# Optimization experiments

Hardware: AMD Instinct MI355X
Metric: run time of the kernel (lower is better)

Reference implementation:

```python
import jax, jax.numpy as jnp
import numpy as np

TRAJ_NUM = 8
EVAL = 30
SGM_T = 2.0
D0 = 0.5
R = 0.3
VOX = 0.2


def setup_inputs() -> dict:
    key = jax.random.key(0)
    ks = jax.random.split(key, 6)
    G, M = 256, 4
    B = G * TRAJ_NUM
    nx, ny, nz = 400, 400, 64
    # quintic boundary matrix at t=0 and t=T; L = A^{-1}
    T = SGM_T
    A = np.array([
        [1, 0, 0, 0, 0, 0],
        [0, 1, 0, 0, 0, 0],
        [0, 0, 2, 0, 0, 0],
        [1, T, T**2, T**3, T**4, T**5],
        [0, 1, 2*T, 3*T**2, 4*T**3, 5*T**4],
        [0, 0, 2, 6*T, 12*T**2, 20*T**3]], dtype=np.float64)
    L = jnp.asarray(np.linalg.inv(A), dtype=jnp.float32)

    def state(k):
        kp, kv, ka = jax.random.split(k, 3)
        # positions inside the 80m x 80m x 12.8m map, away from borders
        p = jax.random.uniform(kp, (B, 3)) * jnp.array([70.0, 70.0, 10.0]) + jnp.array([5.0, 5.0, 1.0])
        v = jax.random.uniform(kv, (B, 3), minval=-1.0, maxval=1.0)
        a = jax.random.uniform(ka, (B, 3), minval=-0.5, maxval=0.5)
        return jnp.stack([p, v, a], axis=-1)  # (B,3,3): rows=axis, cols=[p,v,a]

    Df = state(ks[0])
    Dp = state(ks[1])
    sdf_maps = jax.random.normal(ks[2], (M, nz, ny, nx), dtype=jnp.float32) * 0.5 + 1.0  # (M,D,H,W)
    min_bounds = jnp.zeros((M, 3), jnp.float32)
    sdf_shapes = jnp.tile(jnp.array([[nx, ny, nz]], jnp.float32), (M, 1))  # (nx,ny,nz)
    map_id = jax.random.randint(ks[3], (G,), 0, M)
    return dict(Df=Df, Dp=Dp, L=L, sdf_maps=sdf_maps, min_bounds=min_bounds,
                sdf_shapes=sdf_shapes, map_id=map_id)


def _distance_cost(pos, map_id, sdf_maps, min_bounds, sdf_shapes):
    # pos: (G,N,3) world coords; replicates get_batch_sdf + grid_sample math
    mb = min_bounds[map_id]                           # (G,3)
    shp = sdf_shapes[map_id].astype(jnp.int32)        # (G,3) = (nx,ny,nz)
    mn = jnp.trunc((pos.min(1) - mb) / VOX).astype(jnp.int32)
    mx = jnp.trunc((pos.max(1) - mb) / VOX).astype(jnp.int32)
    max_spans = (mx - mn).max(0)                      # (3,) shared crop span
    c = (mn + mx) // 2
    mn = c - max_spans // 2 - 5
    mx = c + max_spans // 2 + 5
    nmn = jnp.maximum(mn, 0)
    mx = mx + (nmn - mn)
    mn = nmn
    nmx = jnp.minimum(mx, shp)
    mn = mn - (mx - nmx)
    mx = nmx
    shift = jnp.maximum(-jnp.minimum(mn, 0), 0).max(0)  # per-axis over batch
    mn = mn + shift
    local_origin = mn.astype(pos.dtype) * VOX + mb     # (G,3)
    lshape = mx - mn                                   # (G,3) int, crop size

    grid = (pos - local_origin[:, None, :]) / VOX      # local voxel coords (x,y,z)
    gp = 2.0 * grid / (lshape - 1).astype(pos.dtype)[:, None, :] - 1.0
    valid = jnp.all((gp < 0.99) & (gp > -0.99), axis=-1)  # (G,N)

    # trilinear sample, align_corners=True, zeros padding w.r.t. the crop;
    # crop voxel (i,j,k) == full-map voxel (i,j,k)+mn, so gather from the full map
    l0 = jnp.floor(grid).astype(jnp.int32)
    f = grid - l0
    Dm, Hm, Wm = sdf_maps.shape[1:]
    acc = jnp.zeros(pos.shape[:2], pos.dtype)
    for dx in (0, 1):
        for dy in (0, 1):
            for dz in (0, 1):
                il = l0 + jnp.array([dx, dy, dz], jnp.int32)       # (G,N,3) local corner
                inb = jnp.all((il >= 0) & (il < lshape[:, None, :]), axis=-1)
                ig = il + mn[:, None, :]                            # global voxel index
                gx = jnp.clip(ig[..., 0], 0, Wm - 1)
                gy = jnp.clip(ig[..., 1], 0, Hm - 1)
                gz = jnp.clip(ig[..., 2], 0, Dm - 1)
                val = sdf_maps[map_id[:, None], gz, gy, gx]         # (G,N)
                w = ((f[..., 0] if dx else 1 - f[..., 0]) *
                     (f[..., 1] if dy else 1 - f[..., 1]) *
                     (f[..., 2] if dz else 1 - f[..., 2]))
                acc = acc + jnp.where(inb, w * val, 0.0)
    dist = acc
    cost = jnp.exp(-(dist - D0) / R)
    cost = jnp.where(valid, cost, 0.0)
    return cost, dist


def reference(Df, Dp, L, sdf_maps, min_bounds, sdf_shapes, map_id):
    B = Dp.shape[0]
    # coefficients: per axis, coe = L @ [Df_row, Dp_row]
    d = jnp.concatenate([Df, Dp], axis=-1)          # (B,3,6)
    coe = jnp.einsum('jk,bik->bij', L, d)           # (B,3,6)
    dt = SGM_T / EVAL
    t = jnp.linspace(dt, SGM_T, EVAL)               # (30,)
    tp = t[:, None] ** jnp.arange(6)                # (30,6) Vandermonde
    pos = jnp.einsum('nk,bik->bni', tp, coe)        # (B,30,3)
    G = B // TRAJ_NUM
    pos_batch = pos.reshape(G, TRAJ_NUM * EVAL, 3)  # (G,N,3)
    cost, _ = _distance_cost(pos_batch, map_id, sdf_maps, min_bounds, sdf_shapes)
    cost_colli = (cost * dt).reshape(-1, EVAL).sum(-1)  # (B,)
    return cost_colli
```

## Files before the change

### kernel.cpp

```cpp
#include <hip/hip_runtime.h>
#include <hip/hip_bf16.h>
#include <math.h>

#define TRAJ 8
#define EV   30
#define NPT  (TRAJ*EV)
#define GCONST 256
#define MCONST 4
#define NXM  400
#define NYM  400
#define NZM  64

__device__ __forceinline__ float ldf(const void* p, int idx, int isbf) {
    if (isbf) return __bfloat162float(((const __hip_bfloat16*)p)[idx]);
    return ((const float*)p)[idx];
}

__device__ __forceinline__ void resolve_ms(const void*& minb,
                                           const void*& shapes) {
    if (*(const unsigned*)shapes == 0u) {
        const void* t = minb; minb = shapes; shapes = t;
    }
}

__device__ __forceinline__ int detect_bf16(const void* shapes) {
    return *(const unsigned*)shapes != 0x43C80000u;
}

__device__ __forceinline__ void build_coe(const void* Df, const void* Dp,
                                          const void* L, int g, int isbf,
                                          float* sL, float* scoe, int t) {
#pragma clang fp contract(off)
    if (t < 36) sL[t] = ldf(L, t, isbf);
    __syncthreads();
    if (t < 144) {
        int traj = t / 18, rem = t % 18, i = rem / 6, j = rem % 6;
        int b = g * TRAJ + traj;
        float dv[6];
#pragma unroll
        for (int k = 0; k < 3; ++k) {
            dv[k]     = ldf(Df, b * 9 + i * 3 + k, isbf);
            dv[3 + k] = ldf(Dp, b * 9 + i * 3 + k, isbf);
        }
        float s = 0.f;
#pragma unroll
        for (int k = 0; k < 6; ++k) s = s + sL[j * 6 + k] * dv[k];
        scoe[(traj * 3 + i) * 6 + j] = s;
    }
    __syncthreads();
}

__device__ __forceinline__ void eval_pos(const float* scoe, int traj, int e,
                                         double* p) {
    const double dt   = 2.0 / 30.0;
    const double step = (2.0 - dt) / 29.0;
    double tn = (e == EV - 1) ? 2.0 : dt + (double)e * step;
    double tk = 1.0;
    p[0] = p[1] = p[2] = 0.0;
#pragma unroll
    for (int k = 0; k < 6; ++k) {
        p[0] += tk * (double)scoe[(traj * 3 + 0) * 6 + k];
        p[1] += tk * (double)scoe[(traj * 3 + 1) * 6 + k];
        p[2] += tk * (double)scoe[(traj * 3 + 2) * 6 + k];
        tk *= tn;
    }
}

__global__ __launch_bounds__(256) void k_minmax(
    const void* Df, const void* Dp, const void* L, const void* minb_in,
    const void* shapes_in, const int* map_id, int* groupA) {
    __shared__ float  sL[36];
    __shared__ float  scoe[144];
    __shared__ double smin[3][256];
    __shared__ double smax[3][256];
    const void* minb = minb_in; const void* shapes = shapes_in;
    resolve_ms(minb, shapes);
    int g = blockIdx.x, t = threadIdx.x;
    int isbf = detect_bf16(shapes);
    build_coe(Df, Dp, L, g, isbf, sL, scoe, t);

    double p[3] = {0.0, 0.0, 0.0};
    if (t < NPT) eval_pos(scoe, t / EV, t % EV, p);
#pragma unroll
    for (int i = 0; i < 3; ++i) {
        smin[i][t] = (t < NPT) ? p[i] : 1e300;
        smax[i][t] = (t < NPT) ? p[i] : -1e300;
    }
    for (int off = 128; off; off >>= 1) {
        __syncthreads();
        if (t < off)
#pragma unroll
            for (int i = 0; i < 3; ++i) {
                smin[i][t] = fmin(smin[i][t], smin[i][t + off]);
                smax[i][t] = fmax(smax[i][t], smax[i][t + off]);
            }
    }
    __syncthreads();
    if (t == 0) {
        int mid = min(max(map_id[g], 0), MCONST - 1);
#pragma unroll
        for (int i = 0; i < 3; ++i) {
            double mb = (double)ldf(minb, mid * 3 + i, isbf);
            groupA[g * 8 + i]     = (int)trunc((smin[i][0] - mb) / 0.2);
            groupA[g * 8 + 4 + i] = (int)trunc((smax[i][0] - mb) / 0.2);
        }
    }
}

__global__ __launch_bounds__(256) void k_sample(
    const void* Df, const void* Dp, const void* L, const void* minb_in,
    const void* shapes_in, const int* map_id, const void* sdf,
    const int* groupA, float* out) {
    __shared__ float  sL[36];
    __shared__ float  scoe[144];
    __shared__ double scost[NPT];
    __shared__ int    sWin[GCONST][6];
    __shared__ int    sred[3][256];
    const void* minb = minb_in; const void* shapes = shapes_in;
    resolve_ms(minb, shapes);
    int g = blockIdx.x, t = threadIdx.x;
    int isbf = detect_bf16(shapes);

    int mn0[3], mx0[3];
#pragma unroll
    for (int i = 0; i < 3; ++i) {
        mn0[i] = groupA[t * 8 + i];
        mx0[i] = groupA[t * 8 + 4 + i];
        sred[i][t] = mx0[i] - mn0[i];
    }
    for (int off = 128; off; off >>= 1) {
        __syncthreads();
        if (t < off)
#pragma unroll
            for (int i = 0; i < 3; ++i)
                sred[i][t] = max(sred[i][t], sred[i][t + off]);
    }
    __syncthreads();
    int span[3] = {sred[0][0], sred[1][0], sred[2][0]};
    __syncthreads();

    {
        int mid_t = min(max(map_id[t], 0), MCONST - 1);
#pragma unroll
        for (int i = 0; i < 3; ++i) {
            int c   = (mn0[i] + mx0[i]) >> 1;
            int h   = span[i] >> 1;
            int mn1 = c - h - 5, mx1 = c + h + 5;
            int nmn = mn1 > 0 ? mn1 : 0;
            int mx2 = mx1 + (nmn - mn1);
            int shp = (int)ldf(shapes, mid_t * 3 + i, isbf);
            int nmx = mx2 < shp ? mx2 : shp;
            int mn3 = nmn - (mx2 - nmx);
            sWin[t][i]     = mn3;
            sWin[t][3 + i] = nmx;
            sred[i][t]     = mn3 < 0 ? -mn3 : 0;
        }
    }
    for (int off = 128; off; off >>= 1) {
        __syncthreads();
        if (t < off)
#pragma unroll
            for (int i = 0; i < 3; ++i)
                sred[i][t] = max(sred[i][t], sred[i][t + off]);
    }
    __syncthreads();
    int mnf[3], lsh[3];
#pragma unroll
    for (int i = 0; i < 3; ++i) {
        int m  = sWin[g][i] + sred[i][0];
        mnf[i] = m;
        lsh[i] = sWin[g][3 + i] - m;
    }
    __syncthreads();

    build_coe(Df, Dp, L, g, isbf, sL, scoe, t);

    int mid = min(max(map_id[g], 0), MCONST - 1);
    if (t < NPT) {
        double p[3];
        eval_pos(scoe, t / EV, t % EV, p);
        double f[3];
        int    l0[3];
        bool   valid = true;
#pragma unroll
        for (int i = 0; i < 3; ++i) {
            double mb = (double)ldf(minb, mid * 3 + i, isbf);
            double gr = (p[i] - ((double)mnf[i] * 0.2 + mb)) / 0.2;
            double gp = 2.0 * gr / (double)(lsh[i] - 1) - 1.0;
            valid = valid && (gp < 0.99) && (gp > -0.99);
            double fl = floor(gr);
            l0[i] = (int)fl;
            f[i]  = gr - fl;
        }
        const int mbase = mid * (NZM * NYM * NXM);
        int  idx8[8];
        bool inb8[8];
        double w8[8];
#pragma unroll
        for (int c = 0; c < 8; ++c) {
            int dx = c & 1, dy = (c >> 1) & 1, dz = (c >> 2) & 1;
            int ilx = l0[0] + dx, ily = l0[1] + dy, ilz = l0[2] + dz;
            inb8[c] = (ilx >= 0 && ilx < lsh[0]) && (ily >= 0 && ily < lsh[1])
                   && (ilz >= 0 && ilz < lsh[2]);
            int gx = min(max(ilx + mnf[0], 0), NXM - 1);
            int gy = min(max(ily + mnf[1], 0), NYM - 1);
            int gz = min(max(ilz + mnf[2], 0), NZM - 1);
            idx8[c] = mbase + (gz * NYM + gy) * NXM + gx;
            w8[c] = (dx ? f[0] : 1.0 - f[0]) * (dy ? f[1] : 1.0 - f[1])
                  * (dz ? f[2] : 1.0 - f[2]);
        }
        float v8[8];
#pragma unroll
        for (int c = 0; c < 8; ++c) v8[c] = ldf(sdf, idx8[c], isbf);
        double acc = 0.0;
#pragma unroll
        for (int c = 0; c < 8; ++c)
            if (inb8[c]) acc += w8[c] * (double)v8[c];

        double cost = valid ? exp(-(acc - 0.5) / 0.3) : 0.0;
        scost[t] = cost * (2.0 / 30.0);
    }
    __syncthreads();
    if (t < TRAJ) {
        double s = 0.0;
#pragma unroll
        for (int e = 0; e < EV; ++e) s += scost[t * EV + e];
        out[g * TRAJ + t] = (float)s;
    }
}

extern "C" void kernel_launch(void* const* d_in, const int* in_sizes, int n_in,
                              void* d_out, int out_size, void* d_ws,
                              size_t ws_size, hipStream_t stream) {
    int order[16];
    int n = n_in < 16 ? n_in : 16;
    for (int i = 0; i < n; ++i) order[i] = i;
    for (int i = 1; i < n; ++i) {
        int oi = order[i], j = i - 1;
        while (j >= 0 && in_sizes[order[j]] < in_sizes[oi]) {
            order[j + 1] = order[j]; --j;
        }
        order[j + 1] = oi;
    }
    const void* sdf    = d_in[order[0]];
    const void* Df     = d_in[order[1]];
    const void* Dp     = d_in[order[2]];
    const int*  map_id = (const int*)d_in[order[3]];
    const void* L      = d_in[order[4]];
    const void* minb   = d_in[order[5]];
    const void* shapes = d_in[order[6 < n ? 6 : 5]];

    int* groupA = (int*)d_ws;

    k_minmax<<<GCONST, 256, 0, stream>>>(Df, Dp, L, minb, shapes, map_id,
                                         groupA);
    k_sample<<<GCONST, 256, 0, stream>>>(Df, Dp, L, minb, shapes, map_id, sdf,
                                         groupA, (float*)d_out);
    (void)out_size; (void)ws_size;
}
```

Measured before the change: 217.5 us.

## Fuse minmax and sample kernels via cooperative grid sync, use wave-shuffle reductions

Merges the two kernels into one cooperative launch that uses a grid-wide sync between the per-group bounding-box pass and the sampling pass. Positions are cached in shared memory so they are not recomputed after the sync. Shared-memory tree reductions are replaced by 64-lane shuffle reductions plus a small cross-wave step, which cuts the number of block barriers. The aim is to remove a second launch and redundant coefficient and position work. In exchange it depends on cooperative-launch support, keeps a two-kernel fallback, and pays the cost of a grid barrier.

After: 252.2 us. 16.0% more time.

```diff
diff --git a/kernel.cpp b/kernel.cpp
--- a/kernel.cpp
+++ b/kernel.cpp
@@ -1,6 +1,9 @@
 #include <hip/hip_runtime.h>
 #include <hip/hip_bf16.h>
+#include <hip/hip_cooperative_groups.h>
 #include <math.h>
+
+namespace cg = cooperative_groups;
 
 #define TRAJ 8
 #define EV   30
@@ -66,119 +69,11 @@
     }
 }
 
-__global__ __launch_bounds__(256) void k_minmax(
-    const void* Df, const void* Dp, const void* L, const void* minb_in,
-    const void* shapes_in, const int* map_id, int* groupA) {
-    __shared__ float  sL[36];
-    __shared__ float  scoe[144];
-    __shared__ double smin[3][256];
-    __shared__ double smax[3][256];
-    const void* minb = minb_in; const void* shapes = shapes_in;
-    resolve_ms(minb, shapes);
-    int g = blockIdx.x, t = threadIdx.x;
-    int isbf = detect_bf16(shapes);
-    build_coe(Df, Dp, L, g, isbf, sL, scoe, t);
-
-    double p[3] = {0.0, 0.0, 0.0};
-    if (t < NPT) eval_pos(scoe, t / EV, t % EV, p);
-#pragma unroll
-    for (int i = 0; i < 3; ++i) {
-        smin[i][t] = (t < NPT) ? p[i] : 1e300;
-        smax[i][t] = (t < NPT) ? p[i] : -1e300;
-    }
-    for (int off = 128; off; off >>= 1) {
-        __syncthreads();
-        if (t < off)
-#pragma unroll
-            for (int i = 0; i < 3; ++i) {
-                smin[i][t] = fmin(smin[i][t], smin[i][t + off]);
-                smax[i][t] = fmax(smax[i][t], smax[i][t + off]);
-            }
-    }
-    __syncthreads();
-    if (t == 0) {
-        int mid = min(max(map_id[g], 0), MCONST - 1);
-#pragma unroll
-        for (int i = 0; i < 3; ++i) {
-            double mb = (double)ldf(minb, mid * 3 + i, isbf);
-            groupA[g * 8 + i]     = (int)trunc((smin[i][0] - mb) / 0.2);
-            groupA[g * 8 + 4 + i] = (int)trunc((smax[i][0] - mb) / 0.2);
-        }
-    }
-}
-
-__global__ __launch_bounds__(256) void k_sample(
-    const void* Df, const void* Dp, const void* L, const void* minb_in,
-    const void* shapes_in, const int* map_id, const void* sdf,
-    const int* groupA, float* out) {
-    __shared__ float  sL[36];
-    __shared__ float  scoe[144];
-    __shared__ double scost[NPT];
-    __shared__ int    sWin[GCONST][6];
-    __shared__ int    sred[3][256];
-    const void* minb = minb_in; const void* shapes = shapes_in;
-    resolve_ms(minb, shapes);
-    int g = blockIdx.x, t = threadIdx.x;
-    int isbf = detect_bf16(shapes);
-
-    int mn0[3], mx0[3];
-#pragma unroll
-    for (int i = 0; i < 3; ++i) {
-        mn0[i] = groupA[t * 8 + i];
-        mx0[i] = groupA[t * 8 + 4 + i];
-        sred[i][t] = mx0[i] - mn0[i];
-    }
-    for (int off = 128; off; off >>= 1) {
-        __syncthreads();
-        if (t < off)
-#pragma unroll
-            for (int i = 0; i < 3; ++i)
-                sred[i][t] = max(sred[i][t], sred[i][t + off]);
-    }
-    __syncthreads();
-    int span[3] = {sred[0][0], sred[1][0], sred[2][0]};
-    __syncthreads();
-
-    {
-        int mid_t = min(max(map_id[t], 0), MCONST - 1);
-#pragma unroll
-        for (int i = 0; i < 3; ++i) {
-            int c   = (mn0[i] + mx0[i]) >> 1;
-            int h   = span[i] >> 1;
-            int mn1 = c - h - 5, mx1 = c + h + 5;
-            int nmn = mn1 > 0 ? mn1 : 0;
-            int mx2 = mx1 + (nmn - mn1);
-            int shp = (int)ldf(shapes, mid_t * 3 + i, isbf);
-            int nmx = mx2 < shp ? mx2 : shp;
-            int mn3 = nmn - (mx2 - nmx);
-            sWin[t][i]     = mn3;
-            sWin[t][3 + i] = nmx;
-            sred[i][t]     = mn3 < 0 ? -mn3 : 0;
-        }
-    }
-    for (int off = 128; off; off >>= 1) {
-        __syncthreads();
-        if (t < off)
-#pragma unroll
-            for (int i = 0; i < 3; ++i)
-                sred[i][t] = max(sred[i][t], sred[i][t + off]);
-    }
-    __syncthreads();
-    int mnf[3], lsh[3];
-#pragma unroll
-    for (int i = 0; i < 3; ++i) {
-        int m  = sWin[g][i] + sred[i][0];
-        mnf[i] = m;
-        lsh[i] = sWin[g][3 + i] - m;
-    }
-    __syncthreads();
-
-    build_coe(Df, Dp, L, g, isbf, sL, scoe, t);
-
-    int mid = min(max(map_id[g], 0), MCONST - 1);
+__device__ __forceinline__ void sample_and_reduce(
+    const void* minb, const void* shapes, const void* sdf, int isbf, int mid,
+    int g, int t, const int* mnf, const int* lsh, const double* p,
+    double* scost, float* out) {
     if (t < NPT) {
-        double p[3];
-        eval_pos(scoe, t / EV, t % EV, p);
         double f[3];
         int    l0[3];
         bool   valid = true;
@@ -229,6 +124,262 @@
     }
 }
 
+__global__ __launch_bounds__(256) void k_fused(
+    const void* Df, const void* Dp, const void* L, const void* minb_in,
+    const void* shapes_in, const int* map_id, const void* sdf, int* groupA,
+    float* out) {
+    __shared__ float  sL[36];
+    __shared__ float  scoe[144];
+    __shared__ double spos[NPT][3];
+    __shared__ double sredd[3][2][4];
+    __shared__ int    sWin[GCONST][6];
+    __shared__ int    sredi[3][4];
+    __shared__ double scost[NPT];
+
+    const void* minb = minb_in; const void* shapes = shapes_in;
+    resolve_ms(minb, shapes);
+    int g = blockIdx.x, t = threadIdx.x;
+    int lane = t & 63, wid = t >> 6;
+    int isbf = detect_bf16(shapes);
+
+    build_coe(Df, Dp, L, g, isbf, sL, scoe, t);
+
+    double p[3] = {0.0, 0.0, 0.0};
+    if (t < NPT) {
+        eval_pos(scoe, t / EV, t % EV, p);
+        spos[t][0] = p[0]; spos[t][1] = p[1]; spos[t][2] = p[2];
+    }
+    double mn[3], mx[3];
+#pragma unroll
+    for (int i = 0; i < 3; ++i) {
+        mn[i] = (t < NPT) ? p[i] : 1e300;
+        mx[i] = (t < NPT) ? p[i] : -1e300;
+    }
+#pragma unroll
+    for (int off = 32; off; off >>= 1)
+#pragma unroll
+        for (int i = 0; i < 3; ++i) {
+            mn[i] = fmin(mn[i], __shfl_xor(mn[i], off));
+            mx[i] = fmax(mx[i], __shfl_xor(mx[i], off));
+        }
+    if (lane == 0)
+#pragma unroll
+        for (int i = 0; i < 3; ++i) {
+            sredd[i][0][wid] = mn[i];
+            sredd[i][1][wid] = mx[i];
+        }
+    __syncthreads();
+    if (t == 0) {
+        int mid = min(max(map_id[g], 0), MCONST - 1);
+#pragma unroll
+        for (int i = 0; i < 3; ++i) {
+            double a = fmin(fmin(sredd[i][0][0], sredd[i][0][1]),
+                            fmin(sredd[i][0][2], sredd[i][0][3]));
+            double b = fmax(fmax(sredd[i][1][0], sredd[i][1][1]),
+                            fmax(sredd[i][1][2], sredd[i][1][3]));
+            double mb = (double)ldf(minb, mid * 3 + i, isbf);
+            groupA[g * 8 + i]     = (int)trunc((a - mb) / 0.2);
+            groupA[g * 8 + 4 + i] = (int)trunc((b - mb) / 0.2);
+        }
+    }
+    cg::this_grid().sync();
+
+    int mn0[3], mx0[3], v[3];
+#pragma unroll
+    for (int i = 0; i < 3; ++i) {
+        mn0[i] = groupA[t * 8 + i];
+        mx0[i] = groupA[t * 8 + 4 + i];
+        v[i]   = mx0[i] - mn0[i];
+    }
+#pragma unroll
+    for (int off = 32; off; off >>= 1)
+#pragma unroll
+        for (int i = 0; i < 3; ++i) v[i] = max(v[i], __shfl_xor(v[i], off));
+    if (lane == 0)
+#pragma unroll
+        for (int i = 0; i < 3; ++i) sredi[i][wid] = v[i];
+    __syncthreads();
+    int span[3];
+#pragma unroll
+    for (int i = 0; i < 3; ++i)
+        span[i] = max(max(sredi[i][0], sredi[i][1]),
+                      max(sredi[i][2], sredi[i][3]));
+    __syncthreads();
+
+    {
+        int mid_t = min(max(map_id[t], 0), MCONST - 1);
+#pragma unroll
+        for (int i = 0; i < 3; ++i) {
+            int c   = (mn0[i] + mx0[i]) >> 1;
+            int h   = span[i] >> 1;
+            int mn1 = c - h - 5, mx1 = c + h + 5;
+            int nmn = mn1 > 0 ? mn1 : 0;
+            int mx2 = mx1 + (nmn - mn1);
+            int shp = (int)ldf(shapes, mid_t * 3 + i, isbf);
+            int nmx = mx2 < shp ? mx2 : shp;
+            int mn3 = nmn - (mx2 - nmx);
+            sWin[t][i]     = mn3;
+            sWin[t][3 + i] = nmx;
+            v[i]           = mn3 < 0 ? -mn3 : 0;
+        }
+    }
+#pragma unroll
+    for (int off = 32; off; off >>= 1)
+#pragma unroll
+        for (int i = 0; i < 3; ++i) v[i] = max(v[i], __shfl_xor(v[i], off));
+    if (lane == 0)
+#pragma unroll
+        for (int i = 0; i < 3; ++i) sredi[i][wid] = v[i];
+    __syncthreads();
+    int mnf[3], lsh[3];
+#pragma unroll
+    for (int i = 0; i < 3; ++i) {
+        int shift = max(max(sredi[i][0], sredi[i][1]),
+                        max(sredi[i][2], sredi[i][3]));
+        int m  = sWin[g][i] + shift;
+        mnf[i] = m;
+        lsh[i] = sWin[g][3 + i] - m;
+    }
+
+    int mid = min(max(map_id[g], 0), MCONST - 1);
+    double pp[3] = {0.0, 0.0, 0.0};
+    if (t < NPT) { pp[0] = spos[t][0]; pp[1] = spos[t][1]; pp[2] = spos[t][2]; }
+    sample_and_reduce(minb, shapes, sdf, isbf, mid, g, t, mnf, lsh, pp, scost,
+                      out);
+}
+
+__global__ __launch_bounds__(256) void k_minmax(
+    const void* Df, const void* Dp, const void* L, const void* minb_in,
+    const void* shapes_in, const int* map_id, int* groupA) {
+    __shared__ float  sL[36];
+    __shared__ float  scoe[144];
+    __shared__ double sredd[3][2][4];
+    const void* minb = minb_in; const void* shapes = shapes_in;
+    resolve_ms(minb, shapes);
+    int g = blockIdx.x, t = threadIdx.x;
+    int lane = t & 63, wid = t >> 6;
+    int isbf = detect_bf16(shapes);
+    build_coe(Df, Dp, L, g, isbf, sL, scoe, t);
+
+    double p[3] = {0.0, 0.0, 0.0};
+    if (t < NPT) eval_pos(scoe, t / EV, t % EV, p);
+    double mn[3], mx[3];
+#pragma unroll
+    for (int i = 0; i < 3; ++i) {
+        mn[i] = (t < NPT) ? p[i] : 1e300;
+        mx[i] = (t < NPT) ? p[i] : -1e300;
+    }
+#pragma unroll
+    for (int off = 32; off; off >>= 1)
+#pragma unroll
+        for (int i = 0; i < 3; ++i) {
+            mn[i] = fmin(mn[i], __shfl_xor(mn[i], off));
+            mx[i] = fmax(mx[i], __shfl_xor(mx[i], off));
+        }
+    if (lane == 0)
+#pragma unroll
+        for (int i = 0; i < 3; ++i) {
+            sredd[i][0][wid] = mn[i];
+            sredd[i][1][wid] = mx[i];
+        }
+    __syncthreads();
+    if (t == 0) {
+        int mid = min(max(map_id[g], 0), MCONST - 1);
+#pragma unroll
+        for (int i = 0; i < 3; ++i) {
+            double a = fmin(fmin(sredd[i][0][0], sredd[i][0][1]),
+                            fmin(sredd[i][0][2], sredd[i][0][3]));
+            double b = fmax(fmax(sredd[i][1][0], sredd[i][1][1]),
+                            fmax(sredd[i][1][2], sredd[i][1][3]));
+            double mb = (double)ldf(minb, mid * 3 + i, isbf);
+            groupA[g * 8 + i]     = (int)trunc((a - mb) / 0.2);
+            groupA[g * 8 + 4 + i] = (int)trunc((b - mb) / 0.2);
+        }
+    }
+}
+
+__global__ __launch_bounds__(256) void k_sample(
+    const void* Df, const void* Dp, const void* L, const void* minb_in,
+    const void* shapes_in, const int* map_id, const void* sdf,
+    const int* groupA, float* out) {
+    __shared__ float  sL[36];
+    __shared__ float  scoe[144];
+    __shared__ double scost[NPT];
+    __shared__ int    sWin[GCONST][6];
+    __shared__ int    sredi[3][4];
+    const void* minb = minb_in; const void* shapes = shapes_in;
+    resolve_ms(minb, shapes);
+    int g = blockIdx.x, t = threadIdx.x;
+    int lane = t & 63, wid = t >> 6;
+    int isbf = detect_bf16(shapes);
+
+    int mn0[3], mx0[3], v[3];
+#pragma unroll
+    for (int i = 0; i < 3; ++i) {
+        mn0[i] = groupA[t * 8 + i];
+        mx0[i] = groupA[t * 8 + 4 + i];
+        v[i]   = mx0[i] - mn0[i];
+    }
+#pragma unroll
+    for (int off = 32; off; off >>= 1)
+#pragma unroll
+        for (int i = 0; i < 3; ++i) v[i] = max(v[i], __shfl_xor(v[i], off));
+    if (lane == 0)
+#pragma unroll
+        for (int i = 0; i < 3; ++i) sredi[i][wid] = v[i];
+    __syncthreads();
+    int span[3];
+#pragma unroll
+    for (int i = 0; i < 3; ++i)
+        span[i] = max(max(sredi[i][0], sredi[i][1]),
+                      max(sredi[i][2], sredi[i][3]));
+    __syncthreads();
+
+    {
+        int mid_t = min(max(map_id[t], 0), MCONST - 1);
+#pragma unroll
+        for (int i = 0; i < 3; ++i) {
+            int c   = (mn0[i] + mx0[i]) >> 1;
+            int h   = span[i] >> 1;
+            int mn1 = c - h - 5, mx1 = c + h + 5;
+            int nmn = mn1 > 0 ? mn1 : 0;
+            int mx2 = mx1 + (nmn - mn1);
+            int shp = (int)ldf(shapes, mid_t * 3 + i, isbf);
+            int nmx = mx2 < shp ? mx2 : shp;
+            int mn3 = nmn - (mx2 - nmx);
+            sWin[t][i]     = mn3;
+            sWin[t][3 + i] = nmx;
+            v[i]           = mn3 < 0 ? -mn3 : 0;
+        }
+    }
+#pragma unroll
+    for (int off = 32; off; off >>= 1)
+#pragma unroll
+        for (int i = 0; i < 3; ++i) v[i] = max(v[i], __shfl_xor(v[i], off));
+    if (lane == 0)
+#pragma unroll
+        for (int i = 0; i < 3; ++i) sredi[i][wid] = v[i];
+    __syncthreads();
+    int mnf[3], lsh[3];
+#pragma unroll
+    for (int i = 0; i < 3; ++i) {
+        int shift = max(max(sredi[i][0], sredi[i][1]),
+                        max(sredi[i][2], sredi[i][3]));
+        int m  = sWin[g][i] + shift;
+        mnf[i] = m;
+        lsh[i] = sWin[g][3 + i] - m;
+    }
+    __syncthreads();
+
+    build_coe(Df, Dp, L, g, isbf, sL, scoe, t);
+
+    int mid = min(max(map_id[g], 0), MCONST - 1);
+    double p[3] = {0.0, 0.0, 0.0};
+    if (t < NPT) eval_pos(scoe, t / EV, t % EV, p);
+    sample_and_reduce(minb, shapes, sdf, isbf, mid, g, t, mnf, lsh, p, scost,
+                      out);
+}
+
 extern "C" void kernel_launch(void* const* d_in, const int* in_sizes, int n_in,
                               void* d_out, int out_size, void* d_ws,
                               size_t ws_size, hipStream_t stream) {
@@ -251,10 +402,33 @@
     const void* shapes = d_in[order[6 < n ? 6 : 5]];
 
     int* groupA = (int*)d_ws;
-
+    float* outp = (float*)d_out;
+
+    static int coop = -1;
+    if (coop < 0) {
+        int dev = 0;
+        (void)hipGetDevice(&dev);
+        int v = 0;
+        if (hipDeviceGetAttribute(&v, hipDeviceAttributeCooperativeLaunch,
+                                  dev) != hipSuccess)
+            v = 0;
+        coop = v;
+    }
+
+    if (coop) {
+        void* kargs[] = {(void*)&Df,     (void*)&Dp,  (void*)&L,
+                         (void*)&minb,   (void*)&shapes, (void*)&map_id,
+                         (void*)&sdf,    (void*)&groupA, (void*)&outp};
+        if (hipLaunchCooperativeKernel(k_fused, dim3(GCONST), dim3(256), kargs,
+                                       0, stream) == hipSuccess) {
+            (void)out_size; (void)ws_size;
+            return;
+        }
+        coop = 0;
+    }
     k_minmax<<<GCONST, 256, 0, stream>>>(Df, Dp, L, minb, shapes, map_id,
                                          groupA);
     k_sample<<<GCONST, 256, 0, stream>>>(Df, Dp, L, minb, shapes, map_id, sdf,
-                                         groupA, (float*)d_out);
+                                         groupA, outp);
     (void)out_size; (void)ws_size;
 }
```

## Use wavefront shuffle reductions and cache positions between minmax and sample kernels

Applied to the files above, without the earlier changes.

The shared-memory tree reductions in both kernels are replaced with 64-lane wavefront xor-shuffle reductions plus a small cross-wave step, which removes most barriers. The first kernel also writes the evaluated double-precision positions to workspace, so the second kernel can load them instead of rebuilding coefficients and re-evaluating the polynomial whenever the workspace is large enough. The aim is to cut barrier and recompute overhead in these small, latency-bound kernels. In exchange it adds global writes and reads of the position buffer and depends on the workspace size.

Result: no change. 215.7 us (median of 2 runs) (-0.8%).

```diff
diff --git a/kernel.cpp b/kernel.cpp
--- a/kernel.cpp
+++ b/kernel.cpp
@@ -66,119 +66,11 @@
     }
 }
 
-__global__ __launch_bounds__(256) void k_minmax(
-    const void* Df, const void* Dp, const void* L, const void* minb_in,
-    const void* shapes_in, const int* map_id, int* groupA) {
-    __shared__ float  sL[36];
-    __shared__ float  scoe[144];
-    __shared__ double smin[3][256];
-    __shared__ double smax[3][256];
-    const void* minb = minb_in; const void* shapes = shapes_in;
-    resolve_ms(minb, shapes);
-    int g = blockIdx.x, t = threadIdx.x;
-    int isbf = detect_bf16(shapes);
-    build_coe(Df, Dp, L, g, isbf, sL, scoe, t);
-
-    double p[3] = {0.0, 0.0, 0.0};
-    if (t < NPT) eval_pos(scoe, t / EV, t % EV, p);
-#pragma unroll
-    for (int i = 0; i < 3; ++i) {
-        smin[i][t] = (t < NPT) ? p[i] : 1e300;
-        smax[i][t] = (t < NPT) ? p[i] : -1e300;
-    }
-    for (int off = 128; off; off >>= 1) {
-        __syncthreads();
-        if (t < off)
-#pragma unroll
-            for (int i = 0; i < 3; ++i) {
-                smin[i][t] = fmin(smin[i][t], smin[i][t + off]);
-                smax[i][t] = fmax(smax[i][t], smax[i][t + off]);
-            }
-    }
-    __syncthreads();
-    if (t == 0) {
-        int mid = min(max(map_id[g], 0), MCONST - 1);
-#pragma unroll
-        for (int i = 0; i < 3; ++i) {
-            double mb = (double)ldf(minb, mid * 3 + i, isbf);
-            groupA[g * 8 + i]     = (int)trunc((smin[i][0] - mb) / 0.2);
-            groupA[g * 8 + 4 + i] = (int)trunc((smax[i][0] - mb) / 0.2);
-        }
-    }
-}
-
-__global__ __launch_bounds__(256) void k_sample(
-    const void* Df, const void* Dp, const void* L, const void* minb_in,
-    const void* shapes_in, const int* map_id, const void* sdf,
-    const int* groupA, float* out) {
-    __shared__ float  sL[36];
-    __shared__ float  scoe[144];
-    __shared__ double scost[NPT];
-    __shared__ int    sWin[GCONST][6];
-    __shared__ int    sred[3][256];
-    const void* minb = minb_in; const void* shapes = shapes_in;
-    resolve_ms(minb, shapes);
-    int g = blockIdx.x, t = threadIdx.x;
-    int isbf = detect_bf16(shapes);
-
-    int mn0[3], mx0[3];
-#pragma unroll
-    for (int i = 0; i < 3; ++i) {
-        mn0[i] = groupA[t * 8 + i];
-        mx0[i] = groupA[t * 8 + 4 + i];
-        sred[i][t] = mx0[i] - mn0[i];
-    }
-    for (int off = 128; off; off >>= 1) {
-        __syncthreads();
-        if (t < off)
-#pragma unroll
-            for (int i = 0; i < 3; ++i)
-                sred[i][t] = max(sred[i][t], sred[i][t + off]);
-    }
-    __syncthreads();
-    int span[3] = {sred[0][0], sred[1][0], sred[2][0]};
-    __syncthreads();
-
-    {
-        int mid_t = min(max(map_id[t], 0), MCONST - 1);
-#pragma unroll
-        for (int i = 0; i < 3; ++i) {
-            int c   = (mn0[i] + mx0[i]) >> 1;
-            int h   = span[i] >> 1;
-            int mn1 = c - h - 5, mx1 = c + h + 5;
-            int nmn = mn1 > 0 ? mn1 : 0;
-            int mx2 = mx1 + (nmn - mn1);
-            int shp = (int)ldf(shapes, mid_t * 3 + i, isbf);
-            int nmx = mx2 < shp ? mx2 : shp;
-            int mn3 = nmn - (mx2 - nmx);
-            sWin[t][i]     = mn3;
-            sWin[t][3 + i] = nmx;
-            sred[i][t]     = mn3 < 0 ? -mn3 : 0;
-        }
-    }
-    for (int off = 128; off; off >>= 1) {
-        __syncthreads();
-        if (t < off)
-#pragma unroll
-            for (int i = 0; i < 3; ++i)
-                sred[i][t] = max(sred[i][t], sred[i][t + off]);
-    }
-    __syncthreads();
-    int mnf[3], lsh[3];
-#pragma unroll
-    for (int i = 0; i < 3; ++i) {
-        int m  = sWin[g][i] + sred[i][0];
-        mnf[i] = m;
-        lsh[i] = sWin[g][3 + i] - m;
-    }
-    __syncthreads();
-
-    build_coe(Df, Dp, L, g, isbf, sL, scoe, t);
-
-    int mid = min(max(map_id[g], 0), MCONST - 1);
+__device__ __forceinline__ void sample_and_reduce(
+    const void* minb, const void* shapes, const void* sdf, int isbf, int mid,
+    int g, int t, const int* mnf, const int* lsh, const double* p,
+    double* scost, float* out) {
     if (t < NPT) {
-        double p[3];
-        eval_pos(scoe, t / EV, t % EV, p);
         double f[3];
         int    l0[3];
         bool   valid = true;
@@ -229,6 +121,151 @@
     }
 }
 
+__global__ __launch_bounds__(256) void k_minmax(
+    const void* Df, const void* Dp, const void* L, const void* minb_in,
+    const void* shapes_in, const int* map_id, int* groupA, double* posbuf) {
+    __shared__ float  sL[36];
+    __shared__ float  scoe[144];
+    __shared__ double sredd[3][2][4];
+    const void* minb = minb_in; const void* shapes = shapes_in;
+    resolve_ms(minb, shapes);
+    int g = blockIdx.x, t = threadIdx.x;
+    int lane = t & 63, wid = t >> 6;
+    int isbf = detect_bf16(shapes);
+    build_coe(Df, Dp, L, g, isbf, sL, scoe, t);
+
+    double p[3] = {0.0, 0.0, 0.0};
+    if (t < NPT) {
+        eval_pos(scoe, t / EV, t % EV, p);
+        if (posbuf) {
+            double* dst = posbuf + (size_t)g * NPT * 3 + (size_t)t * 3;
+            dst[0] = p[0]; dst[1] = p[1]; dst[2] = p[2];
+        }
+    }
+    double mn[3], mx[3];
+#pragma unroll
+    for (int i = 0; i < 3; ++i) {
+        mn[i] = (t < NPT) ? p[i] : 1e300;
+        mx[i] = (t < NPT) ? p[i] : -1e300;
+    }
+#pragma unroll
+    for (int off = 32; off; off >>= 1)
+#pragma unroll
+        for (int i = 0; i < 3; ++i) {
+            mn[i] = fmin(mn[i], __shfl_xor(mn[i], off));
+            mx[i] = fmax(mx[i], __shfl_xor(mx[i], off));
+        }
+    if (lane == 0)
+#pragma unroll
+        for (int i = 0; i < 3; ++i) {
+            sredd[i][0][wid] = mn[i];
+            sredd[i][1][wid] = mx[i];
+        }
+    __syncthreads();
+    if (t == 0) {
+        int mid = min(max(map_id[g], 0), MCONST - 1);
+#pragma unroll
+        for (int i = 0; i < 3; ++i) {
+            double a = fmin(fmin(sredd[i][0][0], sredd[i][0][1]),
+                            fmin(sredd[i][0][2], sredd[i][0][3]));
+            double b = fmax(fmax(sredd[i][1][0], sredd[i][1][1]),
+                            fmax(sredd[i][1][2], sredd[i][1][3]));
+            double mb = (double)ldf(minb, mid * 3 + i, isbf);
+            groupA[g * 8 + i]     = (int)trunc((a - mb) / 0.2);
+            groupA[g * 8 + 4 + i] = (int)trunc((b - mb) / 0.2);
+        }
+    }
+}
+
+template <bool USEPOS>
+__global__ __launch_bounds__(256) void k_sample(
+    const void* Df, const void* Dp, const void* L, const void* minb_in,
+    const void* shapes_in, const int* map_id, const void* sdf,
+    const int* groupA, const double* posbuf, float* out) {
+    __shared__ float  sL[36];
+    __shared__ float  scoe[144];
+    __shared__ double scost[NPT];
+    __shared__ int    sWin[GCONST][6];
+    __shared__ int    sredi[3][4];
+    const void* minb = minb_in; const void* shapes = shapes_in;
+    resolve_ms(minb, shapes);
+    int g = blockIdx.x, t = threadIdx.x;
+    int lane = t & 63, wid = t >> 6;
+    int isbf = detect_bf16(shapes);
+
+    int mn0[3], mx0[3], v[3];
+#pragma unroll
+    for (int i = 0; i < 3; ++i) {
+        mn0[i] = groupA[t * 8 + i];
+        mx0[i] = groupA[t * 8 + 4 + i];
+        v[i]   = mx0[i] - mn0[i];
+    }
+#pragma unroll
+    for (int off = 32; off; off >>= 1)
+#pragma unroll
+        for (int i = 0; i < 3; ++i) v[i] = max(v[i], __shfl_xor(v[i], off));
+    if (lane == 0)
+#pragma unroll
+        for (int i = 0; i < 3; ++i) sredi[i][wid] = v[i];
+    __syncthreads();
+    int span[3];
+#pragma unroll
+    for (int i = 0; i < 3; ++i)
+        span[i] = max(max(sredi[i][0], sredi[i][1]),
+                      max(sredi[i][2], sredi[i][3]));
+    __syncthreads();
+
+    {
+        int mid_t = min(max(map_id[t], 0), MCONST - 1);
+#pragma unroll
+        for (int i = 0; i < 3; ++i) {
+            int c   = (mn0[i] + mx0[i]) >> 1;
+            int h   = span[i] >> 1;
+            int mn1 = c - h - 5, mx1 = c + h + 5;
+            int nmn = mn1 > 0 ? mn1 : 0;
+            int mx2 = mx1 + (nmn - mn1);
+            int shp = (int)ldf(shapes, mid_t * 3 + i, isbf);
+            int nmx = mx2 < shp ? mx2 : shp;
+            int mn3 = nmn - (mx2 - nmx);
+            sWin[t][i]     = mn3;
+            sWin[t][3 + i] = nmx;
+            v[i]           = mn3 < 0 ? -mn3 : 0;
+        }
+    }
+#pragma unroll
+    for (int off = 32; off; off >>= 1)
+#pragma unroll
+        for (int i = 0; i < 3; ++i) v[i] = max(v[i], __shfl_xor(v[i], off));
+    if (lane == 0)
+#pragma unroll
+        for (int i = 0; i < 3; ++i) sredi[i][wid] = v[i];
+    __syncthreads();
+    int mnf[3], lsh[3];
+#pragma unroll
+    for (int i = 0; i < 3; ++i) {
+        int shift = max(max(sredi[i][0], sredi[i][1]),
+                        max(sredi[i][2], sredi[i][3]));
+        int m  = sWin[g][i] + shift;
+        mnf[i] = m;
+        lsh[i] = sWin[g][3 + i] - m;
+    }
+
+    double p[3] = {0.0, 0.0, 0.0};
+    if (USEPOS) {
+        if (t < NPT) {
+            const double* src = posbuf + (size_t)g * NPT * 3 + (size_t)t * 3;
+            p[0] = src[0]; p[1] = src[1]; p[2] = src[2];
+        }
+    } else {
+        build_coe(Df, Dp, L, g, isbf, sL, scoe, t);
+        if (t < NPT) eval_pos(scoe, t / EV, t % EV, p);
+    }
+
+    int mid = min(max(map_id[g], 0), MCONST - 1);
+    sample_and_reduce(minb, shapes, sdf, isbf, mid, g, t, mnf, lsh, p, scost,
+                      out);
+}
+
 extern "C" void kernel_launch(void* const* d_in, const int* in_sizes, int n_in,
                               void* d_out, int out_size, void* d_ws,
                               size_t ws_size, hipStream_t stream) {
@@ -250,11 +287,22 @@
     const void* minb   = d_in[order[5]];
     const void* shapes = d_in[order[6 < n ? 6 : 5]];
 
-    int* groupA = (int*)d_ws;
+    const size_t posOff   = (size_t)GCONST * 8 * sizeof(int);
+    const size_t posBytes = (size_t)GCONST * NPT * 3 * sizeof(double);
+    int*    groupA = (int*)d_ws;
+    bool    usepos = (ws_size >= posOff + posBytes);
+    double* posbuf = usepos ? (double*)((char*)d_ws + posOff) : nullptr;
+    float*  outp   = (float*)d_out;
 
     k_minmax<<<GCONST, 256, 0, stream>>>(Df, Dp, L, minb, shapes, map_id,
-                                         groupA);
-    k_sample<<<GCONST, 256, 0, stream>>>(Df, Dp, L, minb, shapes, map_id, sdf,
-                                         groupA, (float*)d_out);
-    (void)out_size; (void)ws_size;
-}
+                                         groupA, posbuf);
+    if (usepos)
+        k_sample<true><<<GCONST, 256, 0, stream>>>(Df, Dp, L, minb, shapes,
+                                                   map_id, sdf, groupA, posbuf,
+                                                   outp);
+    else
+        k_sample<false><<<GCONST, 256, 0, stream>>>(Df, Dp, L, minb, shapes,
+                                                    map_id, sdf, groupA,
+                                                    nullptr, outp);
+    (void)out_size;
+}
```
